# Optimization experiments

Measured on AMD Instinct MI355X. Metric: run time of the kernel, lower is better.

The kernel has to match this reference:

```python
import jax, jax.numpy as jnp
import numpy as np

H = 20  # num heads; d_head = 1280 // 20 = 64


def setup_inputs() -> dict:
    key = jax.random.key(0)
    ks = jax.random.split(key, 7)
    B, S, C = 1, 2304, 1280
    hidden_states = jax.random.normal(ks[0], (B, S, C), dtype=jnp.float32)
    # structured boolean sparsity mask (True = keep); force diagonal True so no row is fully masked
    mask = jax.random.randint(ks[1], (S, S), 0, 2) > 0
    mask = mask | jnp.eye(S, dtype=bool)
    w_scale = 0.02  # keep logits in a sane range
    Wq = jax.random.normal(ks[2], (C, C), dtype=jnp.float32) * w_scale
    Wk = jax.random.normal(ks[3], (C, C), dtype=jnp.float32) * w_scale
    Wv = jax.random.normal(ks[4], (C, C), dtype=jnp.float32) * w_scale
    Wo = jax.random.normal(ks[5], (C, C), dtype=jnp.float32) * w_scale
    bo = jnp.zeros((C,), dtype=jnp.float32)
    return {"hidden_states": hidden_states, "mask": mask, "Wq": Wq, "Wk": Wk, "Wv": Wv, "Wo": Wo, "bo": bo}


def reference(hidden_states, mask, Wq, Wk, Wv, Wo, bo):
    B, S, C = hidden_states.shape
    d = C // H
    scale = 1.0 / jnp.sqrt(jnp.float32(d))
    # additive mask: masked_fill(mask == False, -inf)
    add_mask = jnp.where(mask, jnp.float32(0.0), -jnp.inf)  # [S, S]
    # projections (bias-free to_q/to_k/to_v as in diffusers)
    q = hidden_states @ Wq  # [B, S, C]
    k = hidden_states @ Wk
    v = hidden_states @ Wv
    # head_to_batch_dim: [B, S, C] -> [B, H, S, d]
    q = q.reshape(B, S, H, d).transpose(0, 2, 1, 3)
    k = k.reshape(B, S, H, d).transpose(0, 2, 1, 3)
    v = v.reshape(B, S, H, d).transpose(0, 2, 1, 3)
    # get_attention_scores: baddbmm(mask, q, k^T, alpha=scale, beta=1) then softmax
    scores = jnp.einsum("bhqd,bhkd->bhqk", q, k) * scale + add_mask
    probs = jax.nn.softmax(scores, axis=-1)  # [B, H, S, S]
    out = jnp.einsum("bhqk,bhkd->bhqd", probs, v)  # [B, H, S, d]
    # batch_to_head_dim: [B, H, S, d] -> [B, S, C]
    out = out.transpose(0, 2, 1, 3).reshape(B, S, C)
    # to_out[0] Linear + to_out[1] Dropout(eval = identity)
    out = out @ Wo + bo
    return out
```

## Files before the change

kernel.cpp:

```cpp
#include <hip/hip_runtime.h>
#include <stdint.h>

typedef __attribute__((ext_vector_type(8))) short short8;
typedef __attribute__((ext_vector_type(4))) float f32x4;
typedef __attribute__((ext_vector_type(4))) unsigned int u32x4;
typedef unsigned short u16;
typedef unsigned int u32;

#define SEQ  2304
#define CDIM 1280
#define NH   20
#define DH   64
#define MW   72
#define SCL  0.18033688011112043f

__device__ __forceinline__ u16 f2bf(float x){
  u32 u = __builtin_bit_cast(u32, x);
  u += 0x7fffu + ((u >> 16) & 1u);
  return (u16)(u >> 16);
}
__device__ __forceinline__ float bf2f(u16 x){
  u32 u = ((u32)x) << 16;
  return __builtin_bit_cast(float, u);
}

__device__ __forceinline__ u32 cvtpk(float lo, float hi){
  u32 r;
  asm("v_cvt_pk_bf16_f32 %0, %1, %2" : "=v"(r) : "v"(lo), "v"(hi));
  return r;
}

__device__ __forceinline__ void gload16(const void* g, void* l){
  auto gp = (const u32 __attribute__((address_space(1)))*)(uintptr_t)g;
  auto lp = (u32 __attribute__((address_space(3)))*)(uintptr_t)l;
  __builtin_amdgcn_global_load_lds(gp, lp, 16, 0, 0);
}

__global__ __launch_bounds__(256) void k_prep(
    const float* __restrict__ X, const int* __restrict__ Mk,
    const float* __restrict__ w0, const float* __restrict__ w1,
    const float* __restrict__ w2, const float* __restrict__ w3,
    u16* __restrict__ Xb, u32* __restrict__ mb,
    u16* __restrict__ o0, u16* __restrict__ o1,
    u16* __restrict__ o2, u16* __restrict__ o3){
  __shared__ u16 t[64][65];
  int b = blockIdx.x, tid = threadIdx.x;
  if (b < 1440){
    int i = (b*256 + tid)*8;
    float4 v0 = *(const float4*)(X + i);
    float4 v1 = *(const float4*)(X + i + 4);
    short8 o;
    o[0]=(short)f2bf(v0.x); o[1]=(short)f2bf(v0.y); o[2]=(short)f2bf(v0.z); o[3]=(short)f2bf(v0.w);
    o[4]=(short)f2bf(v1.x); o[5]=(short)f2bf(v1.y); o[6]=(short)f2bf(v1.z); o[7]=(short)f2bf(v1.w);
    *(short8*)(Xb + i) = o;
  } else if (b < 3040){
    int b2 = b - 1440;
    int z = b2 / 400, xy = b2 % 400;
    const float* w = z==0?w0: z==1?w1: z==2?w2: w3;
    u16* o        = z==0?o0: z==1?o1: z==2?o2: o3;
    int bx = (xy % 20)*64, by = (xy / 20)*64;
    #pragma unroll
    for (int i = 0; i < 16; i++){
      int idx = tid + i*256; int r = idx>>6, c = idx&63;
      t[r][c] = f2bf(w[(size_t)(by+r)*CDIM + bx + c]);
    }
    __syncthreads();
    #pragma unroll
    for (int i = 0; i < 16; i++){
      int idx = tid + i*256; int r = idx>>6, c = idx&63;
      o[(size_t)(bx+r)*CDIM + by + c] = t[c][r];
    }
  } else {
    int b3 = b - 3040;
    int lane = tid & 63;
    #pragma unroll 4
    for (int it = 0; it < 32; it++){
      int f = (b3*32 + it)*256 + tid;
      unsigned long long bal = __ballot(Mk[f] != 0);
      if ((lane & 31) == 0) mb[f >> 5] = (u32)(bal >> (lane & 32));
    }
  }
}

__global__ __launch_bounds__(256) void k_vt(const u16* __restrict__ v, u16* __restrict__ vt){
  __shared__ u16 t[64][65];
  int bx = blockIdx.x*64, by = blockIdx.y*64, tid = threadIdx.x;
  #pragma unroll
  for (int i = 0; i < 16; i++){
    int idx = tid + i*256; int r = idx>>6, c = idx&63;
    t[r][c] = v[(size_t)(by+r)*CDIM + bx + c];
  }
  if (tid < 64) vt[((size_t)blockIdx.x*80 + 64)*SEQ + by + tid] = 0x3F80;
  __syncthreads();
  #pragma unroll
  for (int i = 0; i < 16; i++){
    int idx = tid + i*256; int r = idx>>6, c = idx&63;
    int s = by + c;
    int x = s & 127;
    int nx = ((x>>5)<<5) | (((x>>2)&3)<<3) | (((x>>4)&1)<<2) | (x&3);
    vt[((size_t)blockIdx.x*80 + r)*SEQ + (s & ~127) + nx] = t[c][r];
  }
}

template<int EPI>
__global__ __launch_bounds__(256) void k_gemm(const u16* __restrict__ A,
    const u16* __restrict__ B0, const u16* __restrict__ B1, const u16* __restrict__ B2,
    u16* __restrict__ O0, u16* __restrict__ O1, u16* __restrict__ O2,
    float* __restrict__ OF, const float* __restrict__ bias){
  const u16* B = blockIdx.z==0 ? B0 : blockIdx.z==1 ? B1 : B2;
  u16* O       = blockIdx.z==0 ? O0 : blockIdx.z==1 ? O1 : O2;
  const float qs = (EPI==0 && blockIdx.z==0) ? SCL : 1.0f;
  __shared__ __align__(16) u16 Al[128*32];
  __shared__ __align__(16) u16 Bl[128*32];
  int tid = threadIdx.x, w = tid>>6, l = tid&63, c16 = l&15, g = l>>4;
  int wr = w>>1, wc = w&1;
  int m0 = blockIdx.y*128, n0 = blockIdx.x*128;
  f32x4 acc[4][4] = {};
  for (int kt = 0; kt < CDIM/32; ++kt){
    #pragma unroll
    for (int i = 0; i < 2; i++){
      int c = i*256 + w*64 + l;
      int r = c>>2, gr = c&3, sg = gr ^ ((r>>1)&3);
      gload16(A + (size_t)(m0+r)*CDIM + kt*32 + sg*8, &Al[(i*256 + w*64)*8]);
    }
    #pragma unroll
    for (int i = 0; i < 2; i++){
      int c = i*256 + w*64 + l;
      int r = c>>2, gr = c&3, sg = gr ^ ((r>>1)&3);
      gload16(B + (size_t)(n0+r)*CDIM + kt*32 + sg*8, &Bl[(i*256 + w*64)*8]);
    }
    __syncthreads();
    short8 af[4], bf[4];
    #pragma unroll
    for (int m = 0; m < 4; m++){
      int r = wr*64 + m*16 + c16; int sg = g ^ ((r>>1)&3);
      af[m] = *(const short8*)&Al[r*32 + sg*8];
    }
    #pragma unroll
    for (int n = 0; n < 4; n++){
      int r = wc*64 + n*16 + c16; int sg = g ^ ((r>>1)&3);
      bf[n] = *(const short8*)&Bl[r*32 + sg*8];
    }
    #pragma unroll
    for (int m = 0; m < 4; m++)
      #pragma unroll
      for (int n = 0; n < 4; n++)
        acc[m][n] = __builtin_amdgcn_mfma_f32_16x16x32_bf16(af[m], bf[n], acc[m][n], 0, 0, 0);
    __syncthreads();
  }
  #pragma unroll
  for (int m = 0; m < 4; m++)
    #pragma unroll
    for (int n = 0; n < 4; n++)
      #pragma unroll
      for (int r = 0; r < 4; r++){
        int row = m0 + wr*64 + m*16 + g*4 + r;
        int col = n0 + wc*64 + n*16 + c16;
        float v = acc[m][n][r];
        if constexpr (EPI == 0) O[(size_t)row*CDIM + col] = f2bf(v * qs);
        else                    OF[(size_t)row*CDIM + col] = v + bias[col];
      }
}

__global__ __launch_bounds__(256, 4) void k_attn(const u16* __restrict__ Q, const u16* __restrict__ K,
    const u16* __restrict__ Vt, const u32* __restrict__ mb,
    u16* __restrict__ N0, u16* __restrict__ N1, u16* __restrict__ N2, float* __restrict__ lrb){
  __shared__ __align__(16) u16 Kl[128*64];
  __shared__ __align__(16) u16 Vl[80*128];
  int tid = threadIdx.x, w = tid>>6, l = tid&63, c16 = l&15, g = l>>4;
  int g4 = g*4;
  int q0 = blockIdx.x*64, h = blockIdx.y, z = blockIdx.z;
  short8 qf[2];
  #pragma unroll
  for (int kf = 0; kf < 2; kf++)
    qf[kf] = *(const short8*)&Q[(size_t)(q0 + w*16 + c16)*CDIM + h*DH + kf*32 + g*8];
  const u32* mrow = mb + (size_t)(q0 + w*16 + c16)*MW;
  f32x4 acc[4] = {};
  f32x4 acc5 = {};
  const f32x4 zz = {0.f, 0.f, 0.f, 0.f};
  for (int kt0 = 0; kt0 < 6; ++kt0){
    int kt = z*6 + kt0;
    #pragma unroll
    for (int i = 0; i < 4; i++){
      int c = i*256 + w*64 + l;
      int r = c>>3, gr = c&7, sg = gr ^ (r&7);
      gload16(K + (size_t)(kt*128 + r)*CDIM + h*DH + sg*8, &Kl[(i*256 + w*64)*8]);
    }
    #pragma unroll
    for (int i = 0; i < 5; i++){
      int c = i*256 + w*64 + l;
      int r = c>>4, gr = c&15, sg = gr ^ (r&7);
      gload16(Vt + ((size_t)h*80 + r)*SEQ + kt*128 + sg*8, &Vl[(i*256 + w*64)*8]);
    }
    u32x4 mw4 = *(const u32x4*)(mrow + kt*4);
    __syncthreads();
    f32x4 s[8];
    __builtin_amdgcn_s_setprio(1);
    #pragma unroll
    for (int fj = 0; fj < 8; fj++){
      s[fj] = zz;
      #pragma unroll
      for (int kf = 0; kf < 2; kf++){
        int rk = fj*16 + c16;
        int sg = (kf*4 + g) ^ (rk&7);
        short8 kb = *(const short8*)&Kl[rk*64 + sg*8];
        s[fj] = __builtin_amdgcn_mfma_f32_16x16x32_bf16(kb, qf[kf], s[fj], 0, 0, 0);
      }
    }
    __builtin_amdgcn_s_setprio(0);
    #pragma unroll
    for (int fj = 0; fj < 8; fj++){
      u32 mwsh = mw4[fj>>1] >> (((fj&1)<<4) + g4);
      #pragma unroll
      for (int r = 0; r < 4; r++){
        float sv = (mwsh & (1u<<r)) ? s[fj][r] : -1e30f;
        s[fj][r] = __builtin_exp2f(sv);
      }
    }
    short8 pa[4];
    #pragma unroll
    for (int kf = 0; kf < 4; kf++){
      u32x4 pw;
      pw[0] = cvtpk(s[2*kf  ][0], s[2*kf  ][1]);
      pw[1] = cvtpk(s[2*kf  ][2], s[2*kf  ][3]);
      pw[2] = cvtpk(s[2*kf+1][0], s[2*kf+1][1]);
      pw[3] = cvtpk(s[2*kf+1][2], s[2*kf+1][3]);
      pa[kf] = __builtin_bit_cast(short8, pw);
    }
    __builtin_amdgcn_s_setprio(1);
    #pragma unroll
    for (int fj = 0; fj < 4; fj++)
      #pragma unroll
      for (int kf = 0; kf < 4; kf++){
        int rv = fj*16 + c16;
        int sg = (kf*4 + g) ^ (rv&7);
        short8 vb = *(const short8*)&Vl[rv*128 + sg*8];
        acc[fj] = __builtin_amdgcn_mfma_f32_16x16x32_bf16(pa[kf], vb, acc[fj], 0, 0, 0);
      }
    #pragma unroll
    for (int kf = 0; kf < 4; kf++){
      int rv = 64 + c16;
      int sg = (kf*4 + g) ^ (rv&7);
      short8 vb = *(const short8*)&Vl[rv*128 + sg*8];
      acc5 = __builtin_amdgcn_mfma_f32_16x16x32_bf16(pa[kf], vb, acc5, 0, 0, 0);
    }
    __builtin_amdgcn_s_setprio(0);
    __syncthreads();
  }
  u16* __restrict__ NB = z==0 ? N0 : z==1 ? N1 : N2;
  float inv[4];
  #pragma unroll
  for (int r = 0; r < 4; r++){
    float lrow = __shfl(acc5[r], l & 48);
    inv[r] = lrow > 0.f ? __builtin_amdgcn_rcpf(lrow) : 0.f;
  }
  #pragma unroll
  for (int fj = 0; fj < 4; fj++)
    #pragma unroll
    for (int r = 0; r < 4; r++){
      int row = q0 + w*16 + g4 + r;
      int col = h*DH + fj*16 + c16;
      NB[(size_t)row*CDIM + col] = f2bf(acc[fj][r] * inv[r]);
    }
  if (c16 == 0){
    #pragma unroll
    for (int r = 0; r < 4; r++)
      lrb[((size_t)z*NH + h)*SEQ + q0 + w*16 + g4 + r] = acc5[r];
  }
}

__global__ __launch_bounds__(256) void k_comb(const u16* __restrict__ N0, const u16* __restrict__ N1,
                                              const u16* __restrict__ N2,
                                              const float* __restrict__ lrb, u16* __restrict__ Ab){
  int e = blockIdx.x*256 + threadIdx.x;
  int row = e / 160, c8 = e % 160;
  int h = c8 >> 3;
  float l0 = lrb[(size_t)h*SEQ + row];
  float l1 = lrb[((size_t)NH + h)*SEQ + row];
  float l2 = lrb[((size_t)2*NH + h)*SEQ + row];
  float ws = __builtin_amdgcn_rcpf(l0 + l1 + l2);
  float w0 = l0*ws, w1 = l1*ws, w2 = l2*ws;
  size_t base = (size_t)row*CDIM + c8*8;
  short8 a = *(const short8*)(N0 + base);
  short8 b = *(const short8*)(N1 + base);
  short8 c = *(const short8*)(N2 + base);
  short8 o;
  #pragma unroll
  for (int j = 0; j < 8; j++)
    o[j] = (short)f2bf(bf2f((u16)a[j])*w0 + bf2f((u16)b[j])*w1 + bf2f((u16)c[j])*w2);
  *(short8*)(Ab + base) = o;
}

extern "C" void kernel_launch(void* const* d_in, const int* in_sizes, int n_in,
                              void* d_out, int out_size, void* d_ws, size_t ws_size,
                              hipStream_t stream){
  const float* X  = (const float*)d_in[0];
  const int*   Mk = (const int*)  d_in[1];
  const float* Wq = (const float*)d_in[2];
  const float* Wk = (const float*)d_in[3];
  const float* Wv = (const float*)d_in[4];
  const float* Wo = (const float*)d_in[5];
  const float* bo = (const float*)d_in[6];
  float* out = (float*)d_out;
  char* ws = (char*)d_ws;
  const size_t SZ_XB = (size_t)SEQ*CDIM*2;
  const size_t SZ_WT = (size_t)CDIM*CDIM*2;
  const size_t SZ_VT = (size_t)NH*80*SEQ*2;
  u16* Xb  = (u16*)(ws);
  u16* WqT = (u16*)(ws + SZ_XB);
  u16* WkT = (u16*)(ws + SZ_XB + 1*SZ_WT);
  u16* WvT = (u16*)(ws + SZ_XB + 2*SZ_WT);
  u16* WoT = (u16*)(ws + SZ_XB + 3*SZ_WT);
  u16* Qb  = (u16*)(ws + 1*SZ_XB + 4*SZ_WT);
  u16* Kb  = (u16*)(ws + 2*SZ_XB + 4*SZ_WT);
  u16* Vb  = (u16*)(ws + 3*SZ_XB + 4*SZ_WT);
  u16* Vt  = (u16*)(ws + 4*SZ_XB + 4*SZ_WT);
  u32* mbp = (u32*)(ws + 4*SZ_XB + 4*SZ_WT + SZ_VT);
  float* lrb = (float*)(ws + 4*SZ_XB + 4*SZ_WT + SZ_VT + (size_t)SEQ*MW*4);
  u16* N0 = Vb;
  u16* N1 = Xb;
  u16* N2 = WqT;
  u16* Ab = Vt;

  k_prep<<<3688, 256, 0, stream>>>(X, Mk, Wq, Wk, Wv, Wo, Xb, mbp, WqT, WkT, WvT, WoT);
  k_gemm<0><<<dim3(10,18,3), 256, 0, stream>>>(Xb, WqT, WkT, WvT, Qb, Kb, Vb, nullptr, nullptr);
  k_vt<<<dim3(20,36), 256, 0, stream>>>(Vb, Vt);
  k_attn<<<dim3(36,20,3), 256, 0, stream>>>(Qb, Kb, Vt, mbp, N0, N1, N2, lrb);
  k_comb<<<1440, 256, 0, stream>>>(N0, N1, N2, lrb, Ab);
  k_gemm<1><<<dim3(10,18,1), 256, 0, stream>>>(Ab, WoT, WoT, WoT, nullptr, nullptr, nullptr, out, bo);
}
```

Baseline: 242.7 us.

## Double-buffer GEMM LDS tiles and split-K the output projection

The GEMM kernel now uses two LDS buffers and prefetches the next k-tile before computing the current one, removing one barrier per iteration. The output projection is split along K into two halves, doubling the number of blocks to better fill the CUs. Partial fp32 results go into reused workspace and a new reduction kernel adds them with the bias. This trades extra global traffic and a launch for better occupancy and latency hiding.

Result: no change. 245.2 us (+1.0%).

```diff
diff --git a/kernel.cpp b/kernel.cpp
--- a/kernel.cpp
+++ b/kernel.cpp
@@ -102,51 +102,62 @@
   }
 }
 
+#define STG(kt, buf) do{ \
+  _Pragma("unroll") for (int i = 0; i < 2; i++){ \
+    int c = i*256 + w*64 + l; int r = c>>2, gr = c&3, sg = gr ^ ((r>>1)&3); \
+    gload16(A + (size_t)(m0+r)*CDIM + (kt)*32 + sg*8, &Al[buf][(i*256 + w*64)*8]); } \
+  _Pragma("unroll") for (int i = 0; i < 2; i++){ \
+    int c = i*256 + w*64 + l; int r = c>>2, gr = c&3, sg = gr ^ ((r>>1)&3); \
+    gload16(B + (size_t)(n0+r)*CDIM + (kt)*32 + sg*8, &Bl[buf][(i*256 + w*64)*8]); } \
+}while(0)
+
 template<int EPI>
 __global__ __launch_bounds__(256) void k_gemm(const u16* __restrict__ A,
     const u16* __restrict__ B0, const u16* __restrict__ B1, const u16* __restrict__ B2,
     u16* __restrict__ O0, u16* __restrict__ O1, u16* __restrict__ O2,
-    float* __restrict__ OF, const float* __restrict__ bias){
-  const u16* B = blockIdx.z==0 ? B0 : blockIdx.z==1 ? B1 : B2;
-  u16* O       = blockIdx.z==0 ? O0 : blockIdx.z==1 ? O1 : O2;
+    float* __restrict__ OF0, float* __restrict__ OF1){
+  const u16* B; u16* O = nullptr; float* OP = nullptr;
+  int k0, nk;
+  if constexpr (EPI == 0){
+    B = blockIdx.z==0 ? B0 : blockIdx.z==1 ? B1 : B2;
+    O = blockIdx.z==0 ? O0 : blockIdx.z==1 ? O1 : O2;
+    k0 = 0; nk = 40;
+  } else {
+    B = B0; OP = blockIdx.z ? OF1 : OF0;
+    k0 = blockIdx.z*20; nk = 20;
+  }
   const float qs = (EPI==0 && blockIdx.z==0) ? SCL : 1.0f;
-  __shared__ __align__(16) u16 Al[128*32];
-  __shared__ __align__(16) u16 Bl[128*32];
+  __shared__ __align__(16) u16 Al[2][128*32];
+  __shared__ __align__(16) u16 Bl[2][128*32];
   int tid = threadIdx.x, w = tid>>6, l = tid&63, c16 = l&15, g = l>>4;
   int wr = w>>1, wc = w&1;
   int m0 = blockIdx.y*128, n0 = blockIdx.x*128;
   f32x4 acc[4][4] = {};
-  for (int kt = 0; kt < CDIM/32; ++kt){
-    #pragma unroll
-    for (int i = 0; i < 2; i++){
-      int c = i*256 + w*64 + l;
-      int r = c>>2, gr = c&3, sg = gr ^ ((r>>1)&3);
-      gload16(A + (size_t)(m0+r)*CDIM + kt*32 + sg*8, &Al[(i*256 + w*64)*8]);
-    }
-    #pragma unroll
-    for (int i = 0; i < 2; i++){
-      int c = i*256 + w*64 + l;
-      int r = c>>2, gr = c&3, sg = gr ^ ((r>>1)&3);
-      gload16(B + (size_t)(n0+r)*CDIM + kt*32 + sg*8, &Bl[(i*256 + w*64)*8]);
-    }
-    __syncthreads();
+  STG(k0, 0);
+  __syncthreads();
+  int cur = 0;
+  for (int kk = 0; kk < nk; ++kk){
+    if (kk+1 < nk) STG(k0+kk+1, cur^1);
     short8 af[4], bf[4];
     #pragma unroll
     for (int m = 0; m < 4; m++){
       int r = wr*64 + m*16 + c16; int sg = g ^ ((r>>1)&3);
-      af[m] = *(const short8*)&Al[r*32 + sg*8];
+      af[m] = *(const short8*)&Al[cur][r*32 + sg*8];
     }
     #pragma unroll
     for (int n = 0; n < 4; n++){
       int r = wc*64 + n*16 + c16; int sg = g ^ ((r>>1)&3);
-      bf[n] = *(const short8*)&Bl[r*32 + sg*8];
+      bf[n] = *(const short8*)&Bl[cur][r*32 + sg*8];
     }
     #pragma unroll
     for (int m = 0; m < 4; m++)
       #pragma unroll
       for (int n = 0; n < 4; n++)
         acc[m][n] = __builtin_amdgcn_mfma_f32_16x16x32_bf16(af[m], bf[n], acc[m][n], 0, 0, 0);
-    __syncthreads();
+    if (kk+1 < nk){
+      __syncthreads();
+      cur ^= 1;
+    }
   }
   #pragma unroll
   for (int m = 0; m < 4; m++)
@@ -158,8 +169,19 @@
         int col = n0 + wc*64 + n*16 + c16;
         float v = acc[m][n][r];
         if constexpr (EPI == 0) O[(size_t)row*CDIM + col] = f2bf(v * qs);
-        else                    OF[(size_t)row*CDIM + col] = v + bias[col];
+        else                    OP[(size_t)row*CDIM + col] = v;
       }
+}
+
+__global__ __launch_bounds__(256) void k_fin(const float* __restrict__ P0, const float* __restrict__ P1,
+                                             const float* __restrict__ bias, float* __restrict__ out){
+  int i = (blockIdx.x*256 + threadIdx.x)*4;
+  int col = i % CDIM;
+  float4 a = *(const float4*)(P0 + i);
+  float4 b = *(const float4*)(P1 + i);
+  float4 c = *(const float4*)(bias + col);
+  float4 o = {a.x+b.x+c.x, a.y+b.y+c.y, a.z+b.z+c.z, a.w+b.w+c.w};
+  *(float4*)(out + i) = o;
 }
 
 __global__ __launch_bounds__(256, 4) void k_attn(const u16* __restrict__ Q, const u16* __restrict__ K,
@@ -321,11 +343,14 @@
   u16* N1 = Xb;
   u16* N2 = WqT;
   u16* Ab = Vt;
+  float* P0 = (float*)Qb;
+  float* P1 = (float*)ws;
 
   k_prep<<<3688, 256, 0, stream>>>(X, Mk, Wq, Wk, Wv, Wo, Xb, mbp, WqT, WkT, WvT, WoT);
   k_gemm<0><<<dim3(10,18,3), 256, 0, stream>>>(Xb, WqT, WkT, WvT, Qb, Kb, Vb, nullptr, nullptr);
   k_vt<<<dim3(20,36), 256, 0, stream>>>(Vb, Vt);
   k_attn<<<dim3(36,20,3), 256, 0, stream>>>(Qb, Kb, Vt, mbp, N0, N1, N2, lrb);
   k_comb<<<1440, 256, 0, stream>>>(N0, N1, N2, lrb, Ab);
-  k_gemm<1><<<dim3(10,18,1), 256, 0, stream>>>(Ab, WoT, WoT, WoT, nullptr, nullptr, nullptr, out, bo);
-}
+  k_gemm<1><<<dim3(10,18,2), 256, 0, stream>>>(Ab, WoT, WoT, WoT, nullptr, nullptr, nullptr, P0, P1);
+  k_fin<<<2880, 256, 0, stream>>>(P0, P1, bo, out);
+}
```
